# Kernel tuning notes

Measured on AMD Instinct MI355X. Metric: run time of the kernel, lower is better.

Reference implementation:

```python
import jax, jax.numpy as jnp
import numpy as np
import math

B, S, HID = 2, 2048, 1536
H, HD = 12, 128           # num_heads, head_dim
LAT = HID // 8            # latent_dim = 192
ROT = HD // 2             # 64, rotary applied to this half-size subspace


def _make_rotary(seq_len, dim=ROT, base=10000.0):
    # LlamaRotaryEmbedding: inv_freq over dim/2 freqs, emb = cat(sin, cos) -> [1,1,S,dim]
    inv_freq = 1.0 / (base ** (np.arange(0, dim, 2, dtype=np.float32) / dim))
    pos = np.arange(seq_len, dtype=np.float32)
    sincos = np.einsum('i,j->ij', pos, inv_freq)  # [S, dim/2]
    emb = np.concatenate([np.sin(sincos), np.cos(sincos)], axis=-1)  # [S, dim]
    return jnp.asarray(emb)[None, None, :, :]


def setup_inputs() -> dict:
    key = jax.random.key(0)
    ks = jax.random.split(key, 10)
    sd = 0.02
    return {
        'hidden_states': jax.random.normal(ks[0], (B, S, HID), jnp.float32),
        'rotary_emb': _make_rotary(S),
        'W_kv_d':  jax.random.normal(ks[1], (HID, LAT), jnp.float32) * sd,
        'W_q_d':   jax.random.normal(ks[2], (HID, LAT), jnp.float32) * sd,
        'W_k_u':   jax.random.normal(ks[3], (LAT, H * ROT), jnp.float32) * sd,
        'W_q_u':   jax.random.normal(ks[4], (LAT, H * ROT), jnp.float32) * sd,
        'W_v_u':   jax.random.normal(ks[5], (LAT, H * HD), jnp.float32) * sd,
        'W_rope_k': jax.random.normal(ks[6], (HID, HID // 2), jnp.float32) * sd,
        'W_rope_q': jax.random.normal(ks[7], (LAT, HID // 2), jnp.float32) * sd,
        'W_o':     jax.random.normal(ks[8], (HID, HID), jnp.float32) * sd,
    }


def _apply_rope(x, emb):
    # x: [B,S,H,ROT]; emb: [1,1,S,ROT] (cat of sin,cos, each ROT/2)
    half = ROT // 2
    x1, x2 = x[..., :half], x[..., half:]
    sin = emb[..., :half].transpose(0, 2, 1, 3)  # -> [1,S,1,half] to broadcast over heads
    cos = emb[..., half:].transpose(0, 2, 1, 3)
    return jnp.concatenate([x1 * cos - x2 * sin, x1 * sin + x2 * cos], axis=-1)


def reference(hidden_states, rotary_emb, W_kv_d, W_q_d, W_k_u, W_q_u, W_v_u,
              W_rope_k, W_rope_q, W_o):
    b, s, _ = hidden_states.shape
    kv_d = hidden_states @ W_kv_d                       # [B,S,LAT]
    q_d = hidden_states @ W_q_d                         # [B,S,LAT]
    k_c = (kv_d @ W_k_u).reshape(b, s, H, ROT)          # content half of K
    q_c = (q_d @ W_q_u).reshape(b, s, H, ROT)
    v = (kv_d @ W_v_u).reshape(b, s, H, HD)
    k_r = (hidden_states @ W_rope_k).reshape(b, s, H, ROT)
    q_r = (q_d @ W_rope_q).reshape(b, s, H, ROT)
    k_r = _apply_rope(k_r, rotary_emb)
    q_r = _apply_rope(q_r, rotary_emb)
    k = jnp.concatenate([k_c, k_r], axis=-1)            # [B,S,H,HD]
    q = jnp.concatenate([q_c, q_r], axis=-1)

    scores = jnp.einsum('bqhd,bkhd->bhqk', q, k) / math.sqrt(HD)
    causal = jnp.tril(jnp.ones((s, s), dtype=bool))
    scores = jnp.where(causal[None, None], scores, jnp.float32(-1e9))
    probs = jax.nn.softmax(scores, axis=-1)
    attn = jnp.einsum('bhqk,bkhd->bqhd', probs, v).reshape(b, s, HID)
    return attn @ W_o
```

## Files before the change

kernel.cpp:

```cpp
#include <hip/hip_runtime.h>
#include <hip/hip_bf16.h>

#define B_ 2
#define S_ 2048
#define HID_ 1536
#define H_ 12
#define HD_ 128
#define LAT_ 192
#define ROT_ 64
#define M_ (B_*S_)

typedef __hip_bfloat16 bf16;

using short8  = __attribute__((ext_vector_type(8))) short;
using short4v = __attribute__((ext_vector_type(4))) short;
using float4v = __attribute__((ext_vector_type(4))) float;

__device__ __forceinline__ unsigned short f2bf(float f) {
  __hip_bfloat16 h = __float2bfloat16(f);
  unsigned short u; __builtin_memcpy(&u, &h, 2); return u;
}

#define GLDS16(gp, lp) __builtin_amdgcn_global_load_lds( \
    (__attribute__((address_space(1))) void*)(size_t)(gp), \
    (__attribute__((address_space(3))) void*)(lp), 16, 0, 0)

__global__ __launch_bounds__(256)
void fillf_k(float* __restrict__ out, float v, int n)
{
  int i = blockIdx.x*256 + threadIdx.x;
  if (i < n) out[i] = v;
}

__global__ __launch_bounds__(256)
void packA_k(const float* __restrict__ in, bf16* __restrict__ out)
{
  int i = (blockIdx.x*256 + threadIdx.x)*4;
  float4 v = *(const float4*)&in[i];
  short4v o;
  o[0] = (short)f2bf(v.x); o[1] = (short)f2bf(v.y);
  o[2] = (short)f2bf(v.z); o[3] = (short)f2bf(v.w);
  *(short4v*)&out[i] = o;
}

__global__ __launch_bounds__(256)
void packT_k(const float* __restrict__ W, bf16* __restrict__ Wt,
             int Kn, int Nn)
{
  __shared__ float t[32][33];
  const int kb = blockIdx.x*32, nb = blockIdx.y*32;
  const int tx = threadIdx.x & 31, ty = threadIdx.x >> 5;
  #pragma unroll
  for (int i = 0; i < 4; i++)
    t[ty+8*i][tx] = W[(size_t)(kb+ty+8*i)*Nn + nb + tx];
  __syncthreads();
  #pragma unroll
  for (int i = 0; i < 4; i++)
    Wt[(size_t)(nb + ty + 8*i)*Kn + kb + tx] = __float2bfloat16(t[tx][ty+8*i]);
}

__global__ __launch_bounds__(256)
void packT3_k(const float* __restrict__ s0, const float* __restrict__ s1,
              const float* __restrict__ s2, bf16* __restrict__ d0,
              bf16* __restrict__ d1, bf16* __restrict__ d2,
              int Kn, int N0, int N1, int N2)
{
  const float* W; bf16* Wt; int Nn;
  if (blockIdx.z == 0)      { W = s0; Wt = d0; Nn = N0; }
  else if (blockIdx.z == 1) { W = s1; Wt = d1; Nn = N1; }
  else                      { W = s2; Wt = d2; Nn = N2; }
  const int kb = blockIdx.x*32, nb = blockIdx.y*32;
  if (nb >= Nn) return;
  __shared__ float t[32][33];
  const int tx = threadIdx.x & 31, ty = threadIdx.x >> 5;
  #pragma unroll
  for (int i = 0; i < 4; i++)
    t[ty+8*i][tx] = W[(size_t)(kb+ty+8*i)*Nn + nb + tx];
  __syncthreads();
  #pragma unroll
  for (int i = 0; i < 4; i++)
    Wt[(size_t)(nb + ty + 8*i)*Kn + kb + tx] = __float2bfloat16(t[tx][ty+8*i]);
}

template<int CMODE, int BM>
__global__ __launch_bounds__(256)
void gemm_mfma(const bf16* __restrict__ A, const bf16* __restrict__ Bt,
               void* __restrict__ Cv, void* __restrict__ Cv2,
               int Kn, int lda, int ldb, int ldc)
{
  constexpr int MI  = BM/32;
  constexpr int ITA = BM/32;
  __shared__ bf16 As[(size_t)BM*64];
  __shared__ bf16 Bs[128*64];

  const int tid  = threadIdx.x;
  const int lane = tid & 63;
  const int w    = tid >> 6;
  const int col  = lane & 15, quad = lane >> 4;
  const int wr   = w >> 1, wc = w & 1;
  const size_t m0 = (size_t)blockIdx.y * BM;
  const size_t n0 = (size_t)blockIdx.x * 128;

  const bf16* ag[ITA]; const bf16* bg[4];
  #pragma unroll
  for (int it = 0; it < ITA; it++) {
    int c = tid + it*256, row = c >> 3, seg = c & 7;
    ag[it] = A + (m0 + row)*lda + (size_t)((seg ^ (row & 7))*8);
  }
  #pragma unroll
  for (int it = 0; it < 4; it++) {
    int c = tid + it*256, row = c >> 3, seg = c & 7;
    bg[it] = Bt + (n0 + row)*ldb + (size_t)((seg ^ (row & 7))*8);
  }

  float4v acc[MI][4];
  #pragma unroll
  for (int i=0;i<MI;i++)
    #pragma unroll
    for (int j=0;j<4;j++) acc[i][j] = (float4v){0.f,0.f,0.f,0.f};

  for (int k0 = 0; k0 < Kn; k0 += 64) {
    #pragma unroll
    for (int it = 0; it < ITA; it++)
      GLDS16(ag[it] + k0, As + (size_t)(tid + it*256)*8);
    #pragma unroll
    for (int it = 0; it < 4; it++)
      GLDS16(bg[it] + k0, Bs + (size_t)(tid + it*256)*8);
    __syncthreads();

    short8 af[MI][2], bfr[4][2];
    #pragma unroll
    for (int i=0;i<MI;i++) {
      const int ar = wr*(BM/2) + i*16 + col;
      #pragma unroll
      for (int k2=0;k2<2;k2++)
        af[i][k2] = *(const short8*)&As[ar*64 + ((k2*4+quad)^(ar&7))*8];
    }
    #pragma unroll
    for (int j=0;j<4;j++) {
      const int br = wc*64 + j*16 + col;
      #pragma unroll
      for (int k2=0;k2<2;k2++)
        bfr[j][k2] = *(const short8*)&Bs[br*64 + ((k2*4+quad)^(br&7))*8];
    }

    #pragma unroll
    for (int k2=0;k2<2;k2++)
      #pragma unroll
      for (int i=0;i<MI;i++)
        #pragma unroll
        for (int j=0;j<4;j++)
          acc[i][j] = __builtin_amdgcn_mfma_f32_16x16x32_bf16(af[i][k2], bfr[j][k2], acc[i][j], 0,0,0);
    __syncthreads();
  }

  #pragma unroll
  for (int i=0;i<MI;i++) {
    const size_t row0 = m0 + wr*(BM/2) + i*16 + quad*4;
    #pragma unroll
    for (int j=0;j<4;j++) {
      const int c = (int)n0 + wc*64 + j*16 + col;
      #pragma unroll
      for (int r=0;r<4;r++) {
        const size_t row = row0 + r;
        const float v = acc[i][j][r];
        if constexpr (CMODE == 0) {
          ((float*)Cv)[row*ldc + c] = v;
        } else if constexpr (CMODE == 3) {
          if (n0 < 768) ((bf16*)Cv)[row*HID_ + (c>>6)*HD_ + (c&63)] = __float2bfloat16(v);
          else          ((bf16*)Cv2)[row*HID_ + (c-768)] = __float2bfloat16(v);
        } else if constexpr (CMODE == 4) {
          if (n0 < 768) ((bf16*)Cv)[row*HID_ + (c>>6)*HD_ + (c&63)] = __float2bfloat16(v);
          else          ((float*)Cv2)[row*768 + (c-768)] = v;
        } else {
          if (n0 < 384) ((bf16*)Cv)[row*384 + c] = __float2bfloat16(v);
          else          ((float*)Cv2)[row*768 + (c-384)] = v;
        }
      }
    }
  }
}

__global__ __launch_bounds__(256)
void rope_pack(const float* __restrict__ krr, const float* __restrict__ qrr,
               const float* __restrict__ emb,
               bf16* __restrict__ Kf, bf16* __restrict__ Qf)
{
  int idx = blockIdx.x*256 + threadIdx.x;
  int i = idx & 31;
  int hm = idx >> 5;
  int h = hm % H_, m = hm / H_;
  int s = m & (S_-1);
  float sn = emb[(size_t)s*ROT_ + i];
  float cs = emb[(size_t)s*ROT_ + 32 + i];

  const float* kr = krr + (size_t)m*(H_*ROT_) + h*ROT_;
  float x1 = kr[i], x2 = kr[32+i];
  bf16* kd = Kf + ((size_t)m*H_ + h)*HD_ + 64;
  kd[i]    = __float2bfloat16(x1*cs - x2*sn);
  kd[32+i] = __float2bfloat16(x1*sn + x2*cs);

  const float* qr = qrr + (size_t)m*(H_*ROT_) + h*ROT_;
  x1 = qr[i]; x2 = qr[32+i];
  bf16* qd = Qf + ((size_t)m*H_ + h)*HD_ + 64;
  qd[i]    = __float2bfloat16(x1*cs - x2*sn);
  qd[32+i] = __float2bfloat16(x1*sn + x2*cs);
}

__global__ __launch_bounds__(256)
void transV_k(const bf16* __restrict__ vfl, bf16* __restrict__ Vtg)
{
  __shared__ unsigned short t[32][36];
  const int nb = blockIdx.x*32, mb = blockIdx.y*32;
  const int c8 = threadIdx.x & 7, r = threadIdx.x >> 3;
  {
    short4v ld = *(const short4v*)((const unsigned short*)vfl +
                                   (size_t)(mb+r)*HID_ + nb + c8*4);
    #pragma unroll
    for (int k=0;k<4;k++) t[r][c8*4+k] = (unsigned short)ld[k];
  }
  __syncthreads();
  const int b = mb >> 11, s0 = mb & (S_-1);
  const int n = nb + r, hh = n >> 7, d = n & 127;
  short4v st;
  #pragma unroll
  for (int k=0;k<4;k++) st[k] = (short)t[c8*4+k][r];
  *(short4v*)((unsigned short*)Vtg +
              ((size_t)(b*H_+hh)*HD_ + d)*S_ + s0 + c8*4) = st;
}

#define KSTR 136
#define VSTR 72
#define PSTR 72

__global__ __launch_bounds__(256)
void attn_mfma(const bf16* __restrict__ Qf, const bf16* __restrict__ Kf,
               const bf16* __restrict__ Vtg, bf16* __restrict__ at)
{
  const int qt = (S_/64 - 1) - (int)(blockIdx.x / (B_*H_));
  const int bh = blockIdx.x % (B_*H_);
  const int h  = bh % H_, b = bh / H_;
  const int tid  = threadIdx.x;
  const int w    = tid >> 6;
  const int lane = tid & 63;
  const int col  = lane & 15;
  const int quad = lane >> 4;

  __shared__ unsigned short Ks[64*KSTR];
  __shared__ unsigned short Vt[128*VSTR];
  __shared__ unsigned short Ps[4][16*PSTR];

  const int q0  = qt * 64;
  const int q0w = q0 + w*16;

  const unsigned short* Kb = (const unsigned short*)Kf +
      ((size_t)b*S_*H_ + h)*HD_;
  const unsigned short* Vb = (const unsigned short*)Vtg +
      (size_t)(b*H_ + h)*HD_*S_;

  const unsigned short* kgp[4]; unsigned short* kdst[4];
  const unsigned short* vgp[4]; unsigned short* vdst[4];
  #pragma unroll
  for (int it = 0; it < 4; it++) {
    int c = tid + it*256;
    int key = c >> 4, doff = (c & 15)*8;
    kgp[it]  = Kb + (size_t)key*HID_ + doff;
    kdst[it] = &Ks[key*KSTR + doff];
    int d = c >> 3, kg = (c & 7)*8;
    vgp[it]  = Vb + (size_t)d*S_ + kg;
    vdst[it] = &Vt[d*VSTR + kg];
  }

  short8 qf[4];
  {
    const unsigned short* qrow = (const unsigned short*)Qf +
        ((size_t)((size_t)b*S_ + q0w + col)*H_ + h)*HD_;
    #pragma unroll
    for (int kk = 0; kk < 4; kk++)
      qf[kk] = *(const short8*)(qrow + kk*32 + quad*8);
  }

  float4v O[8];
  #pragma unroll
  for (int t=0;t<8;t++) O[t] = (float4v){0.f,0.f,0.f,0.f};
  float m_ln = -1e30f, l_ln = 0.f;

  const float scale = 0.08838834764831845f;
  const int nkb = qt + 1;

  short8 kr[4], vr[4];
  #pragma unroll
  for (int it = 0; it < 4; it++) {
    kr[it] = *(const short8*)kgp[it];
    vr[it] = *(const short8*)vgp[it];
  }

  for (int kb = 0; kb < nkb; kb++) {
    const int k0 = kb * 64;

    #pragma unroll
    for (int it = 0; it < 4; it++) *(short8*)kdst[it] = kr[it];
    #pragma unroll
    for (int it = 0; it < 4; it++) *(short8*)vdst[it] = vr[it];
    __syncthreads();

    if (kb + 1 < nkb) {
      const size_t kn = (size_t)(k0 + 64);
      #pragma unroll
      for (int it = 0; it < 4; it++) {
        kr[it] = *(const short8*)(kgp[it] + kn*HID_);
        vr[it] = *(const short8*)(vgp[it] + kn);
      }
    }

    float4v Sf[4];
    #pragma unroll
    for (int tc=0;tc<4;tc++) Sf[tc] = (float4v){0.f,0.f,0.f,0.f};
    __builtin_amdgcn_s_setprio(1);
    #pragma unroll
    for (int tc = 0; tc < 4; tc++) {
      if (k0 + 16*tc <= q0w + 15) {
        #pragma unroll
        for (int kk = 0; kk < 4; kk++) {
          short8 kfrag = *(const short8*)&Ks[(16*tc+col)*KSTR + 32*kk + quad*8];
          Sf[tc] = __builtin_amdgcn_mfma_f32_16x16x32_bf16(kfrag, qf[kk], Sf[tc], 0,0,0);
        }
      }
    }
    __builtin_amdgcn_s_setprio(0);

    const int qrel = q0w + col - k0;
    float sv[4][4];
    float mt = -1e30f;
    #pragma unroll
    for (int tc = 0; tc < 4; tc++)
      #pragma unroll
      for (int r = 0; r < 4; r++) {
        float s = Sf[tc][r] * scale;
        if (tc*16 + quad*4 + r > qrel) s = -1e30f;
        sv[tc][r] = s;
        mt = fmaxf(mt, s);
      }
    mt = fmaxf(mt, __shfl_xor(mt, 16));
    mt = fmaxf(mt, __shfl_xor(mt, 32));
    const float mnew = fmaxf(m_ln, mt);
    float lt = 0.f;
    #pragma unroll
    for (int tc = 0; tc < 4; tc++)
      #pragma unroll
      for (int r = 0; r < 4; r++) {
        sv[tc][r] = __expf(sv[tc][r] - mnew);
        lt += sv[tc][r];
      }
    lt += __shfl_xor(lt, 16);
    lt += __shfl_xor(lt, 32);
    const float al = __expf(m_ln - mnew);
    l_ln = l_ln * al + lt;
    m_ln = mnew;

    #pragma unroll
    for (int tc = 0; tc < 4; tc++) {
      short4v pw;
      pw[0] = (short)f2bf(sv[tc][0]); pw[1] = (short)f2bf(sv[tc][1]);
      pw[2] = (short)f2bf(sv[tc][2]); pw[3] = (short)f2bf(sv[tc][3]);
      *(short4v*)&Ps[w][col*PSTR + tc*16 + quad*4] = pw;
    }

    float alr[4];
    #pragma unroll
    for (int r = 0; r < 4; r++) alr[r] = __shfl(al, quad*4 + r);
    #pragma unroll
    for (int t = 0; t < 8; t++)
      #pragma unroll
      for (int r = 0; r < 4; r++) O[t][r] *= alr[r];

    __builtin_amdgcn_s_setprio(1);
    #pragma unroll
    for (int ks = 0; ks < 2; ks++) {
      if (k0 + 32*ks <= q0w + 15) {
        short8 pf = *(const short8*)&Ps[w][col*PSTR + 32*ks + quad*8];
        #pragma unroll
        for (int t = 0; t < 8; t++) {
          short8 vf = *(const short8*)&Vt[(16*t + col)*VSTR + 32*ks + quad*8];
          O[t] = __builtin_amdgcn_mfma_f32_16x16x32_bf16(pf, vf, O[t], 0,0,0);
        }
      }
    }
    __builtin_amdgcn_s_setprio(0);
    __syncthreads();
  }

  float lr[4];
  #pragma unroll
  for (int r = 0; r < 4; r++) lr[r] = __shfl(l_ln, quad*4 + r);
  #pragma unroll
  for (int r = 0; r < 4; r++) {
    const float linv = 1.f / lr[r];
    const size_t mq = (size_t)b*S_ + q0w + quad*4 + r;
    bf16* dst = at + mq*HID_ + h*HD_ + col;
    #pragma unroll
    for (int t = 0; t < 8; t++)
      dst[16*t] = __float2bfloat16(O[t][r] * linv);
  }
}

extern "C" void kernel_launch(void* const* d_in, const int* in_sizes, int n_in,
                              void* d_out, int out_size, void* d_ws, size_t ws_size,
                              hipStream_t stream)
{
  float* out = (float*)d_out;

  static const int sz_dict[10] = {6291456,131072,294912,294912,147456,
                                  147456,294912,1179648,147456,2359296};
  int bad = -1;
  if (n_in < 10) bad = 15;
  else {
    for (int i = 0; i < 10; i++)
      if (in_sizes[i] != sz_dict[i]) { bad = i; break; }
  }
  if (bad >= 0) {
    float v = 1.0e6f * (float)(1 + bad);
    if (bad < 10) v += (float)(in_sizes[bad] % 1000000);
    fillf_k<<<(out_size + 255)/256, 256, 0, stream>>>(out, v, out_size);
    return;
  }

  const float* hidden = (const float*)d_in[0];
  const float* emb    = (const float*)d_in[1];
  const float* Wkvd   = (const float*)d_in[2];
  const float* Wqd    = (const float*)d_in[3];
  const float* Wku    = (const float*)d_in[4];
  const float* Wqu    = (const float*)d_in[5];
  const float* Wvu    = (const float*)d_in[6];
  const float* Wrk    = (const float*)d_in[7];
  const float* Wrq    = (const float*)d_in[8];
  const float* Wo     = (const float*)d_in[9];

  char* wp = (char*)d_ws;
  size_t used = 0;
  auto alloc = [&](size_t bytes) -> void* {
    void* p = wp + used;
    used += (bytes + 255) & ~(size_t)255;
    return p;
  };
  bf16*  hb    = (bf16*)alloc((size_t)M_*HID_*2);
  bf16*  dout  = (bf16*)alloc((size_t)M_*384*2);
  float* krr   = (float*)alloc((size_t)M_*(H_*ROT_)*4);
  float* qrr   = (float*)alloc((size_t)M_*(H_*ROT_)*4);
  bf16*  Kf    = (bf16*)alloc((size_t)M_*HID_*2);
  bf16*  Qf    = (bf16*)alloc((size_t)M_*HID_*2);
  bf16*  vfl   = (bf16*)alloc((size_t)M_*HID_*2);
  bf16*  Vtg   = (bf16*)alloc((size_t)B_*H_*HD_*S_*2);
  bf16*  at    = (bf16*)alloc((size_t)M_*HID_*2);
  bf16*  WdkrT = (bf16*)alloc((size_t)1152*HID_*2);
  bf16*  WkvuT = (bf16*)alloc((size_t)2304*LAT_*2);
  bf16*  WqurT = (bf16*)alloc((size_t)1536*LAT_*2);
  bf16*  WoT   = (bf16*)alloc((size_t)HID_*HID_*2);

  if (used > ws_size) {
    fillf_k<<<(out_size + 255)/256, 256, 0, stream>>>(out, 5.0e7f, out_size);
    return;
  }

  packA_k<<<(M_*HID_)/1024, 256, 0, stream>>>(hidden, hb);
  packT3_k<<<dim3(48,24,3), 256, 0, stream>>>(
      Wkvd, Wqd, Wrk,
      WdkrT, WdkrT + (size_t)192*HID_, WdkrT + (size_t)384*HID_,
      HID_, LAT_, LAT_, H_*ROT_);
  packT3_k<<<dim3(6,24,3), 256, 0, stream>>>(
      Wku, Wqu, Wrq,
      WkvuT, WqurT, WqurT + (size_t)768*LAT_,
      LAT_, H_*ROT_, H_*ROT_, H_*ROT_);
  packT_k<<<dim3(6,48),  256, 0, stream>>>(Wvu, WkvuT + (size_t)768*LAT_, LAT_, HID_);
  packT_k<<<dim3(48,48), 256, 0, stream>>>(Wo,  WoT, HID_, HID_);

  gemm_mfma<5,64><<<dim3(9, M_/64),  256, 0, stream>>>(hb,        WdkrT, dout, krr, HID_, HID_, HID_, 0);
  gemm_mfma<3,64><<<dim3(18, M_/64), 256, 0, stream>>>(dout,      WkvuT, Kf,   vfl, LAT_, 384, LAT_, 0);
  gemm_mfma<4,64><<<dim3(12, M_/64), 256, 0, stream>>>(dout+192,  WqurT, Qf,   qrr, LAT_, 384, LAT_, 0);

  rope_pack<<<(M_*H_*32)/256, 256, 0, stream>>>(krr, qrr, emb, Kf, Qf);
  transV_k<<<dim3(HID_/32, M_/32), 256, 0, stream>>>(vfl, Vtg);

  attn_mfma<<<B_*H_*(S_/64), 256, 0, stream>>>(Qf, Kf, Vtg, at);

  gemm_mfma<0,128><<<dim3(HID_/128, M_/128), 256, 0, stream>>>(at, WoT, out, nullptr, HID_, HID_, HID_, HID_);
}
```

Baseline: 285.2 us.

## Fuse input cast, RoPE and V transpose into GEMM epilogues; streamline attention softmax

The first projection GEMM now reads fp32 hidden states and converts them to bf16 on the fly, which removes the separate pack pass. RoPE is applied in the epilogues of the first and Q projection GEMMs, and V is written directly in transposed layout, which removes the rope_pack and transV kernels and their intermediate buffers. The weight pack launches are merged into two four-way kernels. Attention specializes the diagonal block, switches to exp2 with a folded scale, and skips the output rescale when the running max barely moves. The fp32 A path loads through registers instead of async LDS loads, and the transposed V stores are scattered.

New measurement: 266.5 us. -6.6%, faster.

```diff
diff --git a/kernel.cpp b/kernel.cpp
--- a/kernel.cpp
+++ b/kernel.cpp
@@ -33,42 +33,19 @@
 }
 
 __global__ __launch_bounds__(256)
-void packA_k(const float* __restrict__ in, bf16* __restrict__ out)
-{
-  int i = (blockIdx.x*256 + threadIdx.x)*4;
-  float4 v = *(const float4*)&in[i];
-  short4v o;
-  o[0] = (short)f2bf(v.x); o[1] = (short)f2bf(v.y);
-  o[2] = (short)f2bf(v.z); o[3] = (short)f2bf(v.w);
-  *(short4v*)&out[i] = o;
-}
-
-__global__ __launch_bounds__(256)
-void packT_k(const float* __restrict__ W, bf16* __restrict__ Wt,
-             int Kn, int Nn)
-{
-  __shared__ float t[32][33];
-  const int kb = blockIdx.x*32, nb = blockIdx.y*32;
-  const int tx = threadIdx.x & 31, ty = threadIdx.x >> 5;
-  #pragma unroll
-  for (int i = 0; i < 4; i++)
-    t[ty+8*i][tx] = W[(size_t)(kb+ty+8*i)*Nn + nb + tx];
-  __syncthreads();
-  #pragma unroll
-  for (int i = 0; i < 4; i++)
-    Wt[(size_t)(nb + ty + 8*i)*Kn + kb + tx] = __float2bfloat16(t[tx][ty+8*i]);
-}
-
-__global__ __launch_bounds__(256)
-void packT3_k(const float* __restrict__ s0, const float* __restrict__ s1,
-              const float* __restrict__ s2, bf16* __restrict__ d0,
-              bf16* __restrict__ d1, bf16* __restrict__ d2,
-              int Kn, int N0, int N1, int N2)
+void packT4_k(const float* __restrict__ s0, const float* __restrict__ s1,
+              const float* __restrict__ s2, const float* __restrict__ s3,
+              bf16* __restrict__ d0, bf16* __restrict__ d1,
+              bf16* __restrict__ d2, bf16* __restrict__ d3,
+              int Kn, int N0, int N1, int N2, int N3)
 {
   const float* W; bf16* Wt; int Nn;
-  if (blockIdx.z == 0)      { W = s0; Wt = d0; Nn = N0; }
-  else if (blockIdx.z == 1) { W = s1; Wt = d1; Nn = N1; }
-  else                      { W = s2; Wt = d2; Nn = N2; }
+  switch (blockIdx.z) {
+    case 0:  W = s0; Wt = d0; Nn = N0; break;
+    case 1:  W = s1; Wt = d1; Nn = N1; break;
+    case 2:  W = s2; Wt = d2; Nn = N2; break;
+    default: W = s3; Wt = d3; Nn = N3; break;
+  }
   const int kb = blockIdx.x*32, nb = blockIdx.y*32;
   if (nb >= Nn) return;
   __shared__ float t[32][33];
@@ -82,11 +59,11 @@
     Wt[(size_t)(nb + ty + 8*i)*Kn + kb + tx] = __float2bfloat16(t[tx][ty+8*i]);
 }
 
-template<int CMODE, int BM>
+template<int CMODE, int BM, int AF32>
 __global__ __launch_bounds__(256)
-void gemm_mfma(const bf16* __restrict__ A, const bf16* __restrict__ Bt,
+void gemm_mfma(const void* __restrict__ Av, const bf16* __restrict__ Bt,
                void* __restrict__ Cv, void* __restrict__ Cv2,
-               int Kn, int lda, int ldb, int ldc)
+               const float* __restrict__ emb, int Kn, int lda, int ldb, int ldc)
 {
   constexpr int MI  = BM/32;
   constexpr int ITA = BM/32;
@@ -101,17 +78,26 @@
   const size_t m0 = (size_t)blockIdx.y * BM;
   const size_t n0 = (size_t)blockIdx.x * 128;
 
-  const bf16* ag[ITA]; const bf16* bg[4];
-  #pragma unroll
-  for (int it = 0; it < ITA; it++) {
-    int c = tid + it*256, row = c >> 3, seg = c & 7;
-    ag[it] = A + (m0 + row)*lda + (size_t)((seg ^ (row & 7))*8);
-  }
+  const bf16* bg[4];
   #pragma unroll
   for (int it = 0; it < 4; it++) {
     int c = tid + it*256, row = c >> 3, seg = c & 7;
     bg[it] = Bt + (n0 + row)*ldb + (size_t)((seg ^ (row & 7))*8);
   }
+  const bf16* ag[ITA];
+  const float* asrc = nullptr;
+  int arow = 0;
+  if constexpr (AF32) {
+    arow = tid >> 2;
+    const int aseg = tid & 3;
+    asrc = (const float*)Av + (m0 + arow)*lda + aseg*16;
+  } else {
+    #pragma unroll
+    for (int it = 0; it < ITA; it++) {
+      int c = tid + it*256, row = c >> 3, seg = c & 7;
+      ag[it] = (const bf16*)Av + (m0 + row)*lda + (size_t)((seg ^ (row & 7))*8);
+    }
+  }
 
   float4v acc[MI][4];
   #pragma unroll
@@ -120,12 +106,32 @@
     for (int j=0;j<4;j++) acc[i][j] = (float4v){0.f,0.f,0.f,0.f};
 
   for (int k0 = 0; k0 < Kn; k0 += 64) {
-    #pragma unroll
-    for (int it = 0; it < ITA; it++)
-      GLDS16(ag[it] + k0, As + (size_t)(tid + it*256)*8);
     #pragma unroll
     for (int it = 0; it < 4; it++)
       GLDS16(bg[it] + k0, Bs + (size_t)(tid + it*256)*8);
+    if constexpr (AF32) {
+      const int aseg = tid & 3;
+      float4 f0 = *(const float4*)(asrc + k0);
+      float4 f1 = *(const float4*)(asrc + k0 + 4);
+      float4 f2 = *(const float4*)(asrc + k0 + 8);
+      float4 f3 = *(const float4*)(asrc + k0 + 12);
+      short8 h0, h1;
+      h0[0]=(short)f2bf(f0.x); h0[1]=(short)f2bf(f0.y);
+      h0[2]=(short)f2bf(f0.z); h0[3]=(short)f2bf(f0.w);
+      h0[4]=(short)f2bf(f1.x); h0[5]=(short)f2bf(f1.y);
+      h0[6]=(short)f2bf(f1.z); h0[7]=(short)f2bf(f1.w);
+      h1[0]=(short)f2bf(f2.x); h1[1]=(short)f2bf(f2.y);
+      h1[2]=(short)f2bf(f2.z); h1[3]=(short)f2bf(f2.w);
+      h1[4]=(short)f2bf(f3.x); h1[5]=(short)f2bf(f3.y);
+      h1[6]=(short)f2bf(f3.z); h1[7]=(short)f2bf(f3.w);
+      const int sl0 = (aseg*2) ^ (arow & 7), sl1 = (aseg*2+1) ^ (arow & 7);
+      *(short8*)&As[arow*64 + sl0*8] = h0;
+      *(short8*)&As[arow*64 + sl1*8] = h1;
+    } else {
+      #pragma unroll
+      for (int it = 0; it < ITA; it++)
+        GLDS16(ag[it] + k0, As + (size_t)(tid + it*256)*8);
+    }
     __syncthreads();
 
     short8 af[MI][2], bfr[4][2];
@@ -154,79 +160,77 @@
     __syncthreads();
   }
 
-  #pragma unroll
-  for (int i=0;i<MI;i++) {
-    const size_t row0 = m0 + wr*(BM/2) + i*16 + quad*4;
-    #pragma unroll
-    for (int j=0;j<4;j++) {
-      const int c = (int)n0 + wc*64 + j*16 + col;
-      #pragma unroll
-      for (int r=0;r<4;r++) {
-        const size_t row = row0 + r;
-        const float v = acc[i][j][r];
-        if constexpr (CMODE == 0) {
-          ((float*)Cv)[row*ldc + c] = v;
-        } else if constexpr (CMODE == 3) {
-          if (n0 < 768) ((bf16*)Cv)[row*HID_ + (c>>6)*HD_ + (c&63)] = __float2bfloat16(v);
-          else          ((bf16*)Cv2)[row*HID_ + (c-768)] = __float2bfloat16(v);
-        } else if constexpr (CMODE == 4) {
-          if (n0 < 768) ((bf16*)Cv)[row*HID_ + (c>>6)*HD_ + (c&63)] = __float2bfloat16(v);
-          else          ((float*)Cv2)[row*768 + (c-768)] = v;
-        } else {
-          if (n0 < 384) ((bf16*)Cv)[row*384 + c] = __float2bfloat16(v);
-          else          ((float*)Cv2)[row*768 + (c-384)] = v;
-        }
-      }
-    }
-  }
-}
-
-__global__ __launch_bounds__(256)
-void rope_pack(const float* __restrict__ krr, const float* __restrict__ qrr,
-               const float* __restrict__ emb,
-               bf16* __restrict__ Kf, bf16* __restrict__ Qf)
-{
-  int idx = blockIdx.x*256 + threadIdx.x;
-  int i = idx & 31;
-  int hm = idx >> 5;
-  int h = hm % H_, m = hm / H_;
-  int s = m & (S_-1);
-  float sn = emb[(size_t)s*ROT_ + i];
-  float cs = emb[(size_t)s*ROT_ + 32 + i];
-
-  const float* kr = krr + (size_t)m*(H_*ROT_) + h*ROT_;
-  float x1 = kr[i], x2 = kr[32+i];
-  bf16* kd = Kf + ((size_t)m*H_ + h)*HD_ + 64;
-  kd[i]    = __float2bfloat16(x1*cs - x2*sn);
-  kd[32+i] = __float2bfloat16(x1*sn + x2*cs);
-
-  const float* qr = qrr + (size_t)m*(H_*ROT_) + h*ROT_;
-  x1 = qr[i]; x2 = qr[32+i];
-  bf16* qd = Qf + ((size_t)m*H_ + h)*HD_ + 64;
-  qd[i]    = __float2bfloat16(x1*cs - x2*sn);
-  qd[32+i] = __float2bfloat16(x1*sn + x2*cs);
-}
-
-__global__ __launch_bounds__(256)
-void transV_k(const bf16* __restrict__ vfl, bf16* __restrict__ Vtg)
-{
-  __shared__ unsigned short t[32][36];
-  const int nb = blockIdx.x*32, mb = blockIdx.y*32;
-  const int c8 = threadIdx.x & 7, r = threadIdx.x >> 3;
-  {
-    short4v ld = *(const short4v*)((const unsigned short*)vfl +
-                                   (size_t)(mb+r)*HID_ + nb + c8*4);
-    #pragma unroll
-    for (int k=0;k<4;k++) t[r][c8*4+k] = (unsigned short)ld[k];
-  }
-  __syncthreads();
-  const int b = mb >> 11, s0 = mb & (S_-1);
-  const int n = nb + r, hh = n >> 7, d = n & 127;
-  short4v st;
-  #pragma unroll
-  for (int k=0;k<4;k++) st[k] = (short)t[c8*4+k][r];
-  *(short4v*)((unsigned short*)Vtg +
-              ((size_t)(b*H_+hh)*HD_ + d)*S_ + s0 + c8*4) = st;
+  if constexpr (CMODE == 0) {
+    #pragma unroll
+    for (int i=0;i<MI;i++) {
+      const size_t row0 = m0 + wr*(BM/2) + i*16 + quad*4;
+      #pragma unroll
+      for (int j=0;j<4;j++) {
+        const int c = (int)n0 + wc*64 + j*16 + col;
+        #pragma unroll
+        for (int r=0;r<4;r++)
+          ((float*)Cv)[(row0+r)*ldc + c] = acc[i][j][r];
+      }
+    }
+    return;
+  }
+
+  constexpr int RBASE = (CMODE == 5) ? 384 : 768;
+  if ((int)n0 < RBASE) {
+    #pragma unroll
+    for (int i=0;i<MI;i++) {
+      const size_t row0 = m0 + wr*(BM/2) + i*16 + quad*4;
+      #pragma unroll
+      for (int j=0;j<4;j++) {
+        const int c = (int)n0 + wc*64 + j*16 + col;
+        #pragma unroll
+        for (int r=0;r<4;r++) {
+          const float v = acc[i][j][r];
+          if constexpr (CMODE == 5)
+            ((bf16*)Cv)[(row0+r)*384 + c] = __float2bfloat16(v);
+          else
+            ((bf16*)Cv)[(row0+r)*HID_ + (c>>6)*HD_ + (c&63)] = __float2bfloat16(v);
+        }
+      }
+    }
+  } else if constexpr (CMODE == 3) {
+    #pragma unroll
+    for (int i=0;i<MI;i++) {
+      const size_t row0 = m0 + wr*(BM/2) + i*16 + quad*4;
+      const int bb = (int)(row0 >> 11), s = (int)(row0 & (S_-1));
+      #pragma unroll
+      for (int j=0;j<4;j++) {
+        const int cv = (int)n0 - 768 + wc*64 + j*16 + col;
+        const int hh = cv >> 7, d = cv & 127;
+        short4v st;
+        #pragma unroll
+        for (int r=0;r<4;r++) st[r] = (short)f2bf(acc[i][j][r]);
+        *(short4v*)((unsigned short*)Cv2 +
+            ((size_t)(bb*H_+hh)*HD_ + d)*S_ + s) = st;
+      }
+    }
+  } else {
+    const int hh = (((int)n0 - RBASE) >> 6) + wc;
+    #pragma unroll
+    for (int i=0;i<MI;i++) {
+      const size_t row0 = m0 + wr*(BM/2) + i*16 + quad*4;
+      #pragma unroll
+      for (int j=0;j<2;j++) {
+        const int idim = j*16 + col;
+        #pragma unroll
+        for (int r=0;r<4;r++) {
+          const size_t row = row0 + r;
+          const int s = (int)(row & (S_-1));
+          const float sn = emb[(size_t)s*ROT_ + idim];
+          const float cs = emb[(size_t)s*ROT_ + 32 + idim];
+          const float x1 = acc[i][j][r], x2 = acc[i][j+2][r];
+          bf16* dst = (bf16*)Cv2 + (row*H_ + hh)*HD_ + 64 + idim;
+          dst[0]  = __float2bfloat16(x1*cs - x2*sn);
+          dst[32] = __float2bfloat16(x1*sn + x2*cs);
+        }
+      }
+    }
+  }
 }
 
 #define KSTR 136
@@ -285,8 +289,7 @@
   for (int t=0;t<8;t++) O[t] = (float4v){0.f,0.f,0.f,0.f};
   float m_ln = -1e30f, l_ln = 0.f;
 
-  const float scale = 0.08838834764831845f;
-  const int nkb = qt + 1;
+  const float scale2 = 0.08838834764831845f * 1.4426950408889634f;
 
   short8 kr[4], vr[4];
   #pragma unroll
@@ -295,8 +298,9 @@
     vr[it] = *(const short8*)vgp[it];
   }
 
-  for (int kb = 0; kb < nkb; kb++) {
+  for (int kb = 0; kb <= qt; kb++) {
     const int k0 = kb * 64;
+    const bool diag = (kb == qt);
 
     #pragma unroll
     for (int it = 0; it < 4; it++) *(short8*)kdst[it] = kr[it];
@@ -304,7 +308,7 @@
     for (int it = 0; it < 4; it++) *(short8*)vdst[it] = vr[it];
     __syncthreads();
 
-    if (kb + 1 < nkb) {
+    if (!diag) {
       const size_t kn = (size_t)(k0 + 64);
       #pragma unroll
       for (int it = 0; it < 4; it++) {
@@ -317,46 +321,89 @@
     #pragma unroll
     for (int tc=0;tc<4;tc++) Sf[tc] = (float4v){0.f,0.f,0.f,0.f};
     __builtin_amdgcn_s_setprio(1);
-    #pragma unroll
-    for (int tc = 0; tc < 4; tc++) {
-      if (k0 + 16*tc <= q0w + 15) {
+    if (!diag) {
+      #pragma unroll
+      for (int tc = 0; tc < 4; tc++)
         #pragma unroll
         for (int kk = 0; kk < 4; kk++) {
           short8 kfrag = *(const short8*)&Ks[(16*tc+col)*KSTR + 32*kk + quad*8];
           Sf[tc] = __builtin_amdgcn_mfma_f32_16x16x32_bf16(kfrag, qf[kk], Sf[tc], 0,0,0);
         }
+    } else {
+      #pragma unroll
+      for (int tc = 0; tc < 4; tc++) {
+        if (tc <= w) {
+          #pragma unroll
+          for (int kk = 0; kk < 4; kk++) {
+            short8 kfrag = *(const short8*)&Ks[(16*tc+col)*KSTR + 32*kk + quad*8];
+            Sf[tc] = __builtin_amdgcn_mfma_f32_16x16x32_bf16(kfrag, qf[kk], Sf[tc], 0,0,0);
+          }
+        }
       }
     }
     __builtin_amdgcn_s_setprio(0);
 
-    const int qrel = q0w + col - k0;
     float sv[4][4];
-    float mt = -1e30f;
-    #pragma unroll
-    for (int tc = 0; tc < 4; tc++)
-      #pragma unroll
-      for (int r = 0; r < 4; r++) {
-        float s = Sf[tc][r] * scale;
-        if (tc*16 + quad*4 + r > qrel) s = -1e30f;
-        sv[tc][r] = s;
-        mt = fmaxf(mt, s);
-      }
-    mt = fmaxf(mt, __shfl_xor(mt, 16));
-    mt = fmaxf(mt, __shfl_xor(mt, 32));
-    const float mnew = fmaxf(m_ln, mt);
-    float lt = 0.f;
-    #pragma unroll
-    for (int tc = 0; tc < 4; tc++)
-      #pragma unroll
-      for (int r = 0; r < 4; r++) {
-        sv[tc][r] = __expf(sv[tc][r] - mnew);
-        lt += sv[tc][r];
-      }
-    lt += __shfl_xor(lt, 16);
-    lt += __shfl_xor(lt, 32);
-    const float al = __expf(m_ln - mnew);
-    l_ln = l_ln * al + lt;
-    m_ln = mnew;
+    float pmax = -3.0e38f;
+    if (!diag) {
+      #pragma unroll
+      for (int tc = 0; tc < 4; tc++)
+        #pragma unroll
+        for (int r = 0; r < 4; r++) {
+          float s = Sf[tc][r] * scale2;
+          sv[tc][r] = s;
+          pmax = fmaxf(pmax, s);
+        }
+    } else {
+      const int qrel = w*16 + col;
+      #pragma unroll
+      for (int tc = 0; tc < 4; tc++)
+        #pragma unroll
+        for (int r = 0; r < 4; r++) {
+          float s = Sf[tc][r] * scale2;
+          if (tc*16 + quad*4 + r > qrel) s = -3.0e38f;
+          sv[tc][r] = s;
+          pmax = fmaxf(pmax, s);
+        }
+    }
+    pmax = fmaxf(pmax, __shfl_xor(pmax, 16));
+    pmax = fmaxf(pmax, __shfl_xor(pmax, 32));
+
+    if (__all(pmax <= m_ln + 11.0f)) {
+      float lt = 0.f;
+      #pragma unroll
+      for (int tc = 0; tc < 4; tc++)
+        #pragma unroll
+        for (int r = 0; r < 4; r++) {
+          sv[tc][r] = exp2f(sv[tc][r] - m_ln);
+          lt += sv[tc][r];
+        }
+      lt += __shfl_xor(lt, 16);
+      lt += __shfl_xor(lt, 32);
+      l_ln += lt;
+    } else {
+      const float mnew = fmaxf(m_ln, pmax);
+      float lt = 0.f;
+      #pragma unroll
+      for (int tc = 0; tc < 4; tc++)
+        #pragma unroll
+        for (int r = 0; r < 4; r++) {
+          sv[tc][r] = exp2f(sv[tc][r] - mnew);
+          lt += sv[tc][r];
+        }
+      lt += __shfl_xor(lt, 16);
+      lt += __shfl_xor(lt, 32);
+      const float al = exp2f(m_ln - mnew);
+      l_ln = l_ln * al + lt;
+      m_ln = mnew;
+      float alr[4];
+      #pragma unroll
+      for (int r = 0; r < 4; r++) alr[r] = __shfl(al, quad*4 + r);
+      #pragma unroll
+      for (int t = 0; t < 8; t++)
+        #pragma unroll
+        for (int r = 0; r < 4; r++) O[t][r] *= alr[r];
+    }
 
     #pragma unroll
     for (int tc = 0; tc < 4; tc++) {
@@ -366,23 +413,27 @@
       *(short4v*)&Ps[w][col*PSTR + tc*16 + quad*4] = pw;
     }
 
-    float alr[4];
-    #pragma unroll
-    for (int r = 0; r < 4; r++) alr[r] = __shfl(al, quad*4 + r);
-    #pragma unroll
-    for (int t = 0; t < 8; t++)
-      #pragma unroll
-      for (int r = 0; r < 4; r++) O[t][r] *= alr[r];
-
     __builtin_amdgcn_s_setprio(1);
-    #pragma unroll
-    for (int ks = 0; ks < 2; ks++) {
-      if (k0 + 32*ks <= q0w + 15) {
+    if (!diag) {
+      #pragma unroll
+      for (int ks = 0; ks < 2; ks++) {
         short8 pf = *(const short8*)&Ps[w][col*PSTR + 32*ks + quad*8];
         #pragma unroll
         for (int t = 0; t < 8; t++) {
           short8 vf = *(const short8*)&Vt[(16*t + col)*VSTR + 32*ks + quad*8];
           O[t] = __builtin_amdgcn_mfma_f32_16x16x32_bf16(pf, vf, O[t], 0,0,0);
+        }
+      }
+    } else {
+      #pragma unroll
+      for (int ks = 0; ks < 2; ks++) {
+        if (ks == 0 || w >= 2) {
+          short8 pf = *(const short8*)&Ps[w][col*PSTR + 32*ks + quad*8];
+          #pragma unroll
+          for (int t = 0; t < 8; t++) {
+            short8 vf = *(const short8*)&Vt[(16*t + col)*VSTR + 32*ks + quad*8];
+            O[t] = __builtin_amdgcn_mfma_f32_16x16x32_bf16(pf, vf, O[t], 0,0,0);
+          }
         }
       }
     }
@@ -443,13 +494,9 @@
     used += (bytes + 255) & ~(size_t)255;
     return p;
   };
-  bf16*  hb    = (bf16*)alloc((size_t)M_*HID_*2);
   bf16*  dout  = (bf16*)alloc((size_t)M_*384*2);
-  float* krr   = (float*)alloc((size_t)M_*(H_*ROT_)*4);
-  float* qrr   = (float*)alloc((size_t)M_*(H_*ROT_)*4);
   bf16*  Kf    = (bf16*)alloc((size_t)M_*HID_*2);
   bf16*  Qf    = (bf16*)alloc((size_t)M_*HID_*2);
-  bf16*  vfl   = (bf16*)alloc((size_t)M_*HID_*2);
   bf16*  Vtg   = (bf16*)alloc((size_t)B_*H_*HD_*S_*2);
   bf16*  at    = (bf16*)alloc((size_t)M_*HID_*2);
   bf16*  WdkrT = (bf16*)alloc((size_t)1152*HID_*2);
@@ -462,26 +509,20 @@
     return;
   }
 
-  packA_k<<<(M_*HID_)/1024, 256, 0, stream>>>(hidden, hb);
-  packT3_k<<<dim3(48,24,3), 256, 0, stream>>>(
-      Wkvd, Wqd, Wrk,
-      WdkrT, WdkrT + (size_t)192*HID_, WdkrT + (size_t)384*HID_,
-      HID_, LAT_, LAT_, H_*ROT_);
-  packT3_k<<<dim3(6,24,3), 256, 0, stream>>>(
-      Wku, Wqu, Wrq,
-      WkvuT, WqurT, WqurT + (size_t)768*LAT_,
-      LAT_, H_*ROT_, H_*ROT_, H_*ROT_);
-  packT_k<<<dim3(6,48),  256, 0, stream>>>(Wvu, WkvuT + (size_t)768*LAT_, LAT_, HID_);
-  packT_k<<<dim3(48,48), 256, 0, stream>>>(Wo,  WoT, HID_, HID_);
-
-  gemm_mfma<5,64><<<dim3(9, M_/64),  256, 0, stream>>>(hb,        WdkrT, dout, krr, HID_, HID_, HID_, 0);
-  gemm_mfma<3,64><<<dim3(18, M_/64), 256, 0, stream>>>(dout,      WkvuT, Kf,   vfl, LAT_, 384, LAT_, 0);
-  gemm_mfma<4,64><<<dim3(12, M_/64), 256, 0, stream>>>(dout+192,  WqurT, Qf,   qrr, LAT_, 384, LAT_, 0);
-
-  rope_pack<<<(M_*H_*32)/256, 256, 0, stream>>>(krr, qrr, emb, Kf, Qf);
-  transV_k<<<dim3(HID_/32, M_/32), 256, 0, stream>>>(vfl, Vtg);
+  packT4_k<<<dim3(48,48,4), 256, 0, stream>>>(
+      Wkvd, Wqd, Wrk, Wo,
+      WdkrT, WdkrT + (size_t)192*HID_, WdkrT + (size_t)384*HID_, WoT,
+      HID_, LAT_, LAT_, H_*ROT_, HID_);
+  packT4_k<<<dim3(6,48,4), 256, 0, stream>>>(
+      Wku, Wvu, Wqu, Wrq,
+      WkvuT, WkvuT + (size_t)768*LAT_, WqurT, WqurT + (size_t)768*LAT_,
+      LAT_, H_*ROT_, HID_, H_*ROT_, H_*ROT_);
+
+  gemm_mfma<5,64,1><<<dim3(9, M_/64),  256, 0, stream>>>(hidden, WdkrT, dout, Kf, emb, HID_, HID_, HID_, 0);
+  gemm_mfma<3,64,0><<<dim3(18, M_/64), 256, 0, stream>>>(dout,     WkvuT, Kf, Vtg, emb, LAT_, 384, LAT_, 0);
+  gemm_mfma<4,64,0><<<dim3(12, M_/64), 256, 0, stream>>>(dout+192, WqurT, Qf, Qf,  emb, LAT_, 384, LAT_, 0);
 
   attn_mfma<<<B_*H_*(S_/64), 256, 0, stream>>>(Qf, Kf, Vtg, at);
 
-  gemm_mfma<0,128><<<dim3(HID_/128, M_/128), 256, 0, stream>>>(at, WoT, out, nullptr, HID_, HID_, HID_, HID_);
+  gemm_mfma<0,128,0><<<dim3(HID_/128, M_/128), 256, 0, stream>>>(at, WoT, out, nullptr, emb, HID_, HID_, HID_, HID_);
 }
```
